# Kernel tuning notes

Measured on AMD Instinct MI355X. Metric: run time of the kernel, lower is better.

Reference implementation:

```python
import jax, jax.numpy as jnp
import numpy as np

B, S, V, L, H, NH, NL = 4, 256, 64, 10, 128, 8, 3
DH = H // NH
LP1 = L + 1


def setup_inputs() -> dict:
    key = jax.random.key(0)
    ks = jax.random.split(key, 18)
    sc = 1.0 / np.sqrt(H)
    return {
        "x": jax.random.normal(ks[0], (B, S, V), jnp.float32),
        "adjacency_logits": jax.random.normal(ks[1], (V, V, LP1), jnp.float32) * 0.1,
        "var_emb": jax.random.normal(ks[2], (V, H), jnp.float32),
        "temp_emb": jax.random.normal(ks[3], (LP1, H), jnp.float32),
        "mech_W": jax.random.normal(ks[4], (V, NL, H, H), jnp.float32) * sc,
        "mech_b": jax.random.normal(ks[5], (V, NL, H), jnp.float32) * 0.01,
        "ln_g": jnp.ones((V, NL, H), jnp.float32),
        "ln_b": jnp.zeros((V, NL, H), jnp.float32),
        "Wq": jax.random.normal(ks[6], (V, H, H), jnp.float32) * sc,
        "Wk": jax.random.normal(ks[7], (V, H, H), jnp.float32) * sc,
        "Wv": jax.random.normal(ks[8], (V, H, H), jnp.float32) * sc,
        "Wo": jax.random.normal(ks[9], (V, H, H), jnp.float32) * sc,
        "bq": jnp.zeros((V, H), jnp.float32),
        "bk": jnp.zeros((V, H), jnp.float32),
        "bv": jnp.zeros((V, H), jnp.float32),
        "bo": jnp.zeros((V, H), jnp.float32),
        "out_W": jax.random.normal(ks[10], (V, H), jnp.float32) * sc,
        "out_b": jnp.zeros((V,), jnp.float32),
    }


def reference(x, adjacency_logits, var_emb, temp_emb, mech_W, mech_b, ln_g, ln_b,
              Wq, Wk, Wv, Wo, bq, bk, bv, bo, out_W, out_b):
    b, s, v = x.shape
    lp1 = adjacency_logits.shape[-1]
    adj = jax.nn.sigmoid(adjacency_logits)  # (V_src, V_tgt, L+1), soft adjacency

    # xlag[b,t,src,l] = x[b, t-l, src] with zero padding (the shift-pad loop, fused)
    xlag = jnp.stack([jnp.pad(x, ((0, 0), (l, 0), (0, 0)))[:, :s] for l in range(lp1)], axis=-1)

    # causal_input[b,t,tgt,h] = sum_{src,l} xlag * adj[src,tgt,l] * (var_emb[src,h] + temp_emb[l,h])
    A = jnp.einsum('btsl,sil->btis', xlag, adj)   # contracted over lag
    Bl = jnp.einsum('btsl,sil->btil', xlag, adj)  # contracted over source
    z = jnp.einsum('btis,sh->btih', A, var_emb) + jnp.einsum('btil,lh->btih', Bl, temp_emb)  # (B,S,V,H)

    # per-variable causal mechanism: Linear -> LayerNorm -> GELU (dropout = identity at eval)
    eps = 1e-5
    nl = mech_W.shape[1]
    for li in range(nl):
        z = jnp.einsum('btvh,vhk->btvk', z, mech_W[:, li]) + mech_b[:, li]
        mu = z.mean(axis=-1, keepdims=True)
        var = z.var(axis=-1, keepdims=True)
        z = (z - mu) / jnp.sqrt(var + eps) * ln_g[:, li] + ln_b[:, li]
        z = jax.nn.gelu(z, approximate=False)

    # per-variable multi-head self-attention over the sequence axis
    def heads(t):
        return t.reshape(b, s, v, NH, DH)
    q = heads(jnp.einsum('btvh,vhk->btvk', z, Wq) + bq)
    k = heads(jnp.einsum('btvh,vhk->btvk', z, Wk) + bk)
    vv = heads(jnp.einsum('btvh,vhk->btvk', z, Wv) + bv)
    scores = jnp.einsum('bqvnd,bkvnd->bvnqk', q, k) / np.sqrt(DH)  # (B,V,NH,S,S)
    attn = jax.nn.softmax(scores, axis=-1)
    o = jnp.einsum('bvnqk,bkvnd->bqvnd', attn, vv).reshape(b, s, v, NH * DH)
    o = jnp.einsum('btvh,vhk->btvk', o, Wo) + bo

    # per-variable output head Linear(H, 1), concatenated over variables
    predictions = jnp.einsum('btvh,vh->btv', o, out_W) + out_b  # (B,S,V)
    return predictions
```

## Files before the change

kernel.cpp:

```cpp
#include <hip/hip_runtime.h>
#include <math.h>

#define BB   4
#define SS   256
#define VV   64
#define LP1  11
#define HH   128
#define NHH  8
#define DHH  16
#define NLL  3
#define BSZ  1024

typedef unsigned short u16;
typedef unsigned int   u32;
typedef __attribute__((ext_vector_type(8))) short s16x8;
typedef __attribute__((ext_vector_type(4))) float f32x4;

__device__ __forceinline__ float bfbits2f(u32 hi16) {
    u32 i = hi16 << 16; float f; __builtin_memcpy(&f, &i, 4); return f;
}
__device__ __forceinline__ u16 f2bf(float f) {
    u32 i; __builtin_memcpy(&i, &f, 4);
    return (u16)((i + 0x7fffu + ((i >> 16) & 1u)) >> 16);
}
__device__ __forceinline__ u16 f2bf_trunc(float f) {
    u32 i; __builtin_memcpy(&i, &f, 4);
    return (u16)(i >> 16);
}
__device__ __forceinline__ float ldf(const void* p, size_t i, int isbf) {
    if (isbf) return bfbits2f(((const u16*)p)[i]);
    return ((const float*)p)[i];
}
__device__ __forceinline__ float4 ld4(const void* p, size_t i, int isbf) {
    float4 v;
    if (isbf) {
        uint2 u = *(const uint2*)((const u16*)p + i);
        v.x = bfbits2f(u.x & 0xffffu); v.y = bfbits2f(u.x >> 16);
        v.z = bfbits2f(u.y & 0xffffu); v.w = bfbits2f(u.y >> 16);
    } else {
        v = *(const float4*)((const float*)p + i);
    }
    return v;
}
__device__ __forceinline__ void gll16(const u16* g, u16* l) {
    __builtin_amdgcn_global_load_lds(
        (const __attribute__((address_space(1))) void*)g,
        (__attribute__((address_space(3))) void*)l, 16, 0, 0);
}

__global__ __launch_bounds__(64) void k_sniff(const u16* __restrict__ probe,
                                              int* __restrict__ flags) {
    if (threadIdx.x == 0) {
        int wild = 0;
        for (int j = 0; j < 256; j++) {
            float v = bfbits2f(probe[j]);
            if (!(fabsf(v) < 1e8f)) wild = 1;
        }
        flags[0] = wild ? 0 : 1;
    }
}

__global__ __launch_bounds__(256) void k_adj(const void* __restrict__ logits,
                                             float* __restrict__ adj,
                                             const int* __restrict__ flags) {
    int isbf = flags[0];
    int i = blockIdx.x * 256 + threadIdx.x;
    if (i < VV * VV * LP1) {
        float v = ldf(logits, i, isbf);
        adj[i] = 1.f / (1.f + expf(-v));
    }
}

__global__ __launch_bounds__(128) void k_fuse(const void* __restrict__ Wo,
                                              const void* __restrict__ outW,
                                              const void* __restrict__ bo,
                                              const void* __restrict__ outb,
                                              float* __restrict__ wfused,
                                              float* __restrict__ bfused,
                                              const int* __restrict__ flags) {
    int isbf = flags[0];
    int v = blockIdx.x; int h = threadIdx.x;
    __shared__ float ow[HH];
    __shared__ float red[HH];
    ow[h] = ldf(outW, (size_t)v * HH + h, isbf);
    __syncthreads();
    size_t wb = ((size_t)v * HH + h) * HH;
    float acc = 0.f;
    #pragma unroll 8
    for (int k = 0; k < HH; k++) acc += ldf(Wo, wb + k, isbf) * ow[k];
    wfused[v * HH + h] = acc;
    red[h] = ldf(bo, (size_t)v * HH + h, isbf) * ow[h];
    __syncthreads();
    for (int s = 64; s > 0; s >>= 1) { if (h < s) red[h] += red[h + s]; __syncthreads(); }
    if (h == 0) bfused[v] = red[0] + ldf(outb, v, isbf);
}

__global__ __launch_bounds__(256) void k_causal(const void* __restrict__ x,
                                                const float* __restrict__ adj,
                                                const void* __restrict__ var_emb,
                                                const void* __restrict__ temp_emb,
                                                u16* __restrict__ zh,
                                                u16* __restrict__ zl,
                                                const int* __restrict__ flags) {
    __shared__ float xl[LP1][VV];
    __shared__ float A_sh[VV][VV + 1];
    __shared__ float Blp_sh[VV * LP1 * 4];
    __shared__ float Bl_sh[VV][12];
    int isbf = flags[0];
    int tid = threadIdx.x;
    int bt = blockIdx.x; int b = bt >> 8; int t = bt & 255;

    for (int p = tid; p < LP1 * VV; p += 256) {
        int l = p >> 6, s = p & 63; int tt = t - l;
        xl[l][s] = (tt >= 0) ? ldf(x, (size_t)(b * SS + tt) * VV + s, isbf) : 0.f;
    }
    __syncthreads();

    {
        int i = tid & 63, sg = tid >> 6;
        float blp[LP1];
        #pragma unroll
        for (int l = 0; l < LP1; l++) blp[l] = 0.f;
        for (int k = 0; k < 16; k++) {
            int s = sg + k * 4;
            const float* ap = adj + (s * VV + i) * LP1;
            float a = 0.f;
            #pragma unroll
            for (int l = 0; l < LP1; l++) {
                float pr = xl[l][s] * ap[l];
                a += pr; blp[l] += pr;
            }
            A_sh[i][s] = a;
        }
        #pragma unroll
        for (int l = 0; l < LP1; l++)
            Blp_sh[(i * LP1 + l) * 4 + sg] = blp[l];
    }
    __syncthreads();
    for (int p = tid; p < VV * LP1; p += 256) {
        int i = p / LP1, l = p - i * LP1;
        const float* q = &Blp_sh[(i * LP1 + l) * 4];
        Bl_sh[i][l] = (q[0] + q[1]) + (q[2] + q[3]);
    }
    __syncthreads();

    int h0 = (tid & 31) * 4;
    int ig = tid >> 5;
    float acc[8][4];
    #pragma unroll
    for (int ii = 0; ii < 8; ii++)
        #pragma unroll
        for (int j = 0; j < 4; j++) acc[ii][j] = 0.f;

    if (isbf) {
        for (int s = 0; s < VV; s++) {
            float4 v4 = ld4(var_emb, (size_t)s * HH + h0, 1);
            #pragma unroll
            for (int ii = 0; ii < 8; ii++) {
                float a = A_sh[ig * 8 + ii][s];
                acc[ii][0] += a * v4.x; acc[ii][1] += a * v4.y;
                acc[ii][2] += a * v4.z; acc[ii][3] += a * v4.w;
            }
        }
        #pragma unroll
        for (int l = 0; l < LP1; l++) {
            float4 t4 = ld4(temp_emb, (size_t)l * HH + h0, 1);
            #pragma unroll
            for (int ii = 0; ii < 8; ii++) {
                float bl = Bl_sh[ig * 8 + ii][l];
                acc[ii][0] += bl * t4.x; acc[ii][1] += bl * t4.y;
                acc[ii][2] += bl * t4.z; acc[ii][3] += bl * t4.w;
            }
        }
    } else {
        for (int s = 0; s < VV; s++) {
            float4 v4 = ld4(var_emb, (size_t)s * HH + h0, 0);
            #pragma unroll
            for (int ii = 0; ii < 8; ii++) {
                float a = A_sh[ig * 8 + ii][s];
                acc[ii][0] += a * v4.x; acc[ii][1] += a * v4.y;
                acc[ii][2] += a * v4.z; acc[ii][3] += a * v4.w;
            }
        }
        #pragma unroll
        for (int l = 0; l < LP1; l++) {
            float4 t4 = ld4(temp_emb, (size_t)l * HH + h0, 0);
            #pragma unroll
            for (int ii = 0; ii < 8; ii++) {
                float bl = Bl_sh[ig * 8 + ii][l];
                acc[ii][0] += bl * t4.x; acc[ii][1] += bl * t4.y;
                acc[ii][2] += bl * t4.z; acc[ii][3] += bl * t4.w;
            }
        }
    }

    #pragma unroll
    for (int ii = 0; ii < 8; ii++) {
        int i = ig * 8 + ii;
        size_t idx = ((size_t)i * BSZ + bt) * HH + h0;
        u16 h0_ = f2bf(acc[ii][0]), h1_ = f2bf(acc[ii][1]);
        u16 h2_ = f2bf(acc[ii][2]), h3_ = f2bf(acc[ii][3]);
        uint2 hw, lw;
        hw.x = (u32)h0_ | ((u32)h1_ << 16); hw.y = (u32)h2_ | ((u32)h3_ << 16);
        lw.x = (u32)f2bf(acc[ii][0] - bfbits2f(h0_)) | ((u32)f2bf(acc[ii][1] - bfbits2f(h1_)) << 16);
        lw.y = (u32)f2bf(acc[ii][2] - bfbits2f(h2_)) | ((u32)f2bf(acc[ii][3] - bfbits2f(h3_)) << 16);
        *(uint2*)&zh[idx] = hw;
        *(uint2*)&zl[idx] = lw;
    }
}

struct WPack {
    const void* src[4];
    u16* dh[4];
    u16* dl[4];
};
#define TP 136
__global__ __launch_bounds__(256) void k_wprep(WPack wp,
                                               const int* __restrict__ flags) {
    int isbf = flags[0];
    int mat = blockIdx.x;
    int seg = (mat < 192) ? 0 : 1 + ((mat - 192) >> 6);
    int rel = (mat < 192) ? mat : ((mat - 192) & 63);
    const void* raw = wp.src[seg];
    u16* Wh = wp.dh[seg];
    u16* Wl = wp.dl[seg];
    int tid = threadIdx.x;
    size_t src = (size_t)rel * (HH * HH);
    if (isbf) {
        __shared__ u16 tile[HH * TP];
        const uint4* sp = (const uint4*)((const u16*)raw + src);
        #pragma unroll
        for (int u = 0; u < 8; u++) {
            int p = u * 256 + tid;
            int h = p >> 4, k8 = (p & 15) * 8;
            int k8s = k8 ^ ((((u32)h >> 3) & 15) * 8);
            *(uint4*)&tile[h * TP + k8s] = sp[p];
        }
        __syncthreads();
        #pragma unroll
        for (int u = 0; u < 8; u++) {
            int p = u * 256 + tid;
            int kcol = p >> 4, h8 = (p & 15) * 8;
            u16 vals[8];
            #pragma unroll
            for (int j = 0; j < 8; j++) {
                int h = h8 + j;
                int ks = kcol ^ ((((u32)h >> 3) & 15) * 8);
                vals[j] = tile[h * TP + ks];
            }
            uint4 pk;
            pk.x = (u32)vals[0] | ((u32)vals[1] << 16);
            pk.y = (u32)vals[2] | ((u32)vals[3] << 16);
            pk.z = (u32)vals[4] | ((u32)vals[5] << 16);
            pk.w = (u32)vals[6] | ((u32)vals[7] << 16);
            int c = h8 >> 6;
            int kloc = (h8 & 63) ^ ((kcol & 7) * 8);
            *(uint4*)&Wh[src + c * 8192 + kcol * 64 + kloc] = pk;
        }
    } else {
        int kcol = tid >> 1, h0 = (tid & 1) * 64;
        for (int i = 0; i < 64; i++) {
            int h = h0 + i;
            float w = ldf(raw, src + (size_t)h * HH + kcol, 0);
            u16 hi = f2bf(w);
            int c = h >> 6;
            size_t dst = src + c * 8192 + (size_t)kcol * 64 + ((h & 63) ^ ((kcol & 7) * 8));
            Wh[dst] = hi;
            Wl[dst] = f2bf(w - bfbits2f(hi));
        }
    }
}

#define PB  72
__global__ __launch_bounds__(256) void k_mega(
    const u16* __restrict__ zh, const u16* __restrict__ zl,
    const u16* __restrict__ WmH, const u16* __restrict__ WmL,
    const u16* __restrict__ WqH, const u16* __restrict__ WqL,
    const u16* __restrict__ WkH, const u16* __restrict__ WkL,
    const u16* __restrict__ WvH, const u16* __restrict__ WvL,
    const void* __restrict__ mechb,
    const void* __restrict__ lng, const void* __restrict__ lnb,
    const void* __restrict__ bq, const void* __restrict__ bk,
    const void* __restrict__ bv,
    u16* __restrict__ Qh, u16* __restrict__ Ql,
    u16* __restrict__ Ko, u16* __restrict__ Vt,
    const int* __restrict__ flags)
{
    __shared__ u16 Az_h[64 * 128];
    __shared__ u16 Az_l[64 * 128];
    __shared__ u16 Bd_s[2][128 * 64];
    u16* Vt_sh = &Bd_s[0][0];
    int isbf = flags[0];
    int wexact = isbf;
    int tid = threadIdx.x;
    int bid = blockIdx.x;
    int xcd = bid & 7, idx = bid >> 3;
    int v = xcd * 8 + (idx >> 4);
    int tile = idx & 15;
    int wave = tid >> 6, lane = tid & 63;
    int quad = lane >> 4, l15 = lane & 15;
    int m0 = wave * 16;
    int swzl = (l15 & 7) * 8;

    size_t zbase = ((size_t)v * BSZ + (size_t)tile * 64) * HH;

    int shift = wexact ? 1 : 2;
    int PER = 1 << shift;
    int NCH = 6 << shift;

    auto wchunk = [&](int ch) -> const u16* {
        int li = ch >> shift;
        int sub = ch & (PER - 1);
        int cc = sub & 1, lo = sub >> 1;
        const u16* p; size_t wb;
        if (li < 3)       { p = lo ? WmL : WmH; wb = (size_t)(v * NLL + li) * 16384; }
        else if (li == 3) { p = lo ? WqL : WqH; wb = (size_t)v * 16384; }
        else if (li == 4) { p = lo ? WkL : WkH; wb = (size_t)v * 16384; }
        else              { p = lo ? WvL : WvH; wb = (size_t)v * 16384; }
        return p + wb + cc * 8192;
    };
    auto stageB = [&](u16* dst, const u16* g) {
        const u16* gl = g + wave * 2048 + lane * 8;
        u16* lb = dst + wave * 2048;
        #pragma unroll
        for (int u = 0; u < 4; u++)
            gll16(gl + u * 512, lb + u * 512);
    };

    {
        int rl = lane >> 4;
        int kc = (lane & 15) * 8;
        #pragma unroll
        for (int u = 0; u < 4; u++) {
            int row = wave * 16 + u * 4 + rl;
            int kcs = kc ^ ((row & 7) * 8);
            gll16(&zh[zbase + (size_t)row * HH + kcs], &Az_h[(wave * 16 + u * 4) * 128]);
            gll16(&zl[zbase + (size_t)row * HH + kcs], &Az_l[(wave * 16 + u * 4) * 128]);
        }
    }
    stageB(&Bd_s[0][0], wchunk(0));
    __syncthreads();

    f32x4 acc[8];

    auto epilogue = [&](int li) {
        float bcol[8], gcol[8], b2col[8];
        #pragma unroll
        for (int nt = 0; nt < 8; nt++) {
            int col = nt * 16 + l15;
            if (li < 3) {
                size_t pb = (size_t)v * (NLL * HH) + (size_t)li * HH + col;
                bcol[nt]  = ldf(mechb, pb, isbf);
                gcol[nt]  = ldf(lng, pb, isbf);
                b2col[nt] = ldf(lnb, pb, isbf);
            } else {
                const void* bp = (li == 3) ? bq : (li == 4) ? bk : bv;
                bcol[nt] = ldf(bp, (size_t)v * HH + col, isbf);
            }
        }
        if (li == 5) __syncthreads();
        #pragma unroll
        for (int r = 0; r < 4; r++) {
            float vals[8];
            float sum = 0.f, sq = 0.f;
            #pragma unroll
            for (int nt = 0; nt < 8; nt++) {
                float val = acc[nt][r] + bcol[nt];
                vals[nt] = val; sum += val; sq += val * val;
            }
            int rloc = m0 + quad * 4 + r;
            if (li < 3) {
                #pragma unroll
                for (int m = 1; m < 16; m <<= 1) {
                    sum += __shfl_xor(sum, m);
                    sq  += __shfl_xor(sq, m);
                }
                float mean = sum * (1.f / HH);
                float var  = sq * (1.f / HH) - mean * mean;
                float rstd = rsqrtf(var + 1e-5f);
                int swr = (rloc & 7) * 8;
                #pragma unroll
                for (int nt = 0; nt < 8; nt++) {
                    float y = (vals[nt] - mean) * rstd * gcol[nt] + b2col[nt];
                    y = 0.5f * y * (1.f + erff(y * 0.70710678118654752f));
                    u16 hi = f2bf(y);
                    int colw = (nt * 16 + l15) ^ swr;
                    Az_h[rloc * 128 + colw] = hi;
                    Az_l[rloc * 128 + colw] = f2bf(y - bfbits2f(hi));
                }
            } else if (li == 3) {
                int row = tile * 64 + rloc;
                size_t ob = ((size_t)v * BSZ + row) * HH;
                #pragma unroll
                for (int nt = 0; nt < 8; nt++) {
                    u16 hi = f2bf(vals[nt]);
                    Qh[ob + nt * 16 + l15] = hi;
                    Ql[ob + nt * 16 + l15] = f2bf(vals[nt] - bfbits2f(hi));
                }
            } else if (li == 4) {
                int row = tile * 64 + rloc;
                size_t ob = ((size_t)v * BSZ + row) * HH;
                #pragma unroll
                for (int nt = 0; nt < 8; nt++)
                    Ko[ob + nt * 16 + l15] = f2bf(vals[nt]);
            } else {
                #pragma unroll
                for (int nt = 0; nt < 8; nt++)
                    Vt_sh[(nt * 16 + l15) * PB + rloc] = f2bf(vals[nt]);
            }
        }
        if (li == 5) {
            __syncthreads();
            int col = tid >> 1, half = tid & 1;
            int n = col >> 4, d = col & 15;
            int bb = tile >> 2, t0 = (tile & 3) * 64;
            size_t dst = (((size_t)(v * BB + bb) * NHH + n) * DHH + d) * SS + t0 + half * 32;
            #pragma unroll
            for (int j = 0; j < 4; j++)
                *(uint4*)&Vt[dst + j * 8] = *(const uint4*)&Vt_sh[col * PB + half * 32 + j * 8];
        }
    };

    for (int ch = 0; ch < NCH; ch++) {
        int bsel = ch & 1;
        if (ch + 1 < NCH) stageB(&Bd_s[bsel ^ 1][0], wchunk(ch + 1));
        int sub = ch & (PER - 1);
        int li = ch >> shift;
        int cc = sub & 1, lo = sub >> 1;
        if (sub == 0) {
            #pragma unroll
            for (int nt = 0; nt < 8; nt++) {
                f32x4 zz = {0.f, 0.f, 0.f, 0.f};
                acc[nt] = zz;
            }
        }
        const u16* Bp = &Bd_s[bsel][0];
        #pragma unroll
        for (int kk = 0; kk < 2; kk++) {
            int acol = (cc * 64 + kk * 32 + quad * 8) ^ swzl;
            int bcol = (kk * 32 + quad * 8) ^ swzl;
            s16x8 ah = *(const s16x8*)&Az_h[(m0 + l15) * 128 + acol];
            if (!lo) {
                s16x8 al = *(const s16x8*)&Az_l[(m0 + l15) * 128 + acol];
                #pragma unroll
                for (int nt = 0; nt < 8; nt++) {
                    s16x8 bh = *(const s16x8*)&Bp[(nt * 16 + l15) * 64 + bcol];
                    acc[nt] = __builtin_amdgcn_mfma_f32_16x16x32_bf16(ah, bh, acc[nt], 0, 0, 0);
                    acc[nt] = __builtin_amdgcn_mfma_f32_16x16x32_bf16(al, bh, acc[nt], 0, 0, 0);
                }
            } else {
                #pragma unroll
                for (int nt = 0; nt < 8; nt++) {
                    s16x8 bl = *(const s16x8*)&Bp[(nt * 16 + l15) * 64 + bcol];
                    acc[nt] = __builtin_amdgcn_mfma_f32_16x16x32_bf16(ah, bl, acc[nt], 0, 0, 0);
                }
            }
        }
        if (sub == PER - 1) epilogue(li);
        __syncthreads();
    }
}

#define LDW 40
__global__ __launch_bounds__(256) void k_attn2(const u16* __restrict__ Qh,
                                               const u16* __restrict__ Ql,
                                               const u16* __restrict__ K16,
                                               const u16* __restrict__ Vt,
                                               float* __restrict__ O) {
    __shared__ u16 Kp_sh[SS * LDW];
    __shared__ u16 Vt_sh[DHH * 264];
    __shared__ u16 P_sh[4][16 * LDW];
    int tid = threadIdx.x;
    int wave = tid >> 6, lane = tid & 63;
    int quad = lane >> 4, l15 = lane & 15;
    int bn = blockIdx.x, v = blockIdx.y;
    int b = bn >> 3, n = bn & 7;
    size_t qkbase = ((size_t)v * BSZ + b * SS) * HH + n * DHH;
    size_t vtbase = ((size_t)(v * BB + b) * NHH + n) * DHH * SS;

    {
        int row = tid;
        uint4 k0 = *(const uint4*)&K16[qkbase + (size_t)row * HH];
        uint4 k1 = *(const uint4*)&K16[qkbase + (size_t)row * HH + 8];
        *(uint4*)&Kp_sh[row * LDW + 0]  = k0;
        *(uint4*)&Kp_sh[row * LDW + 8]  = k1;
        *(uint4*)&Kp_sh[row * LDW + 16] = k0;
        *(uint4*)&Kp_sh[row * LDW + 24] = k1;
    }
    #pragma unroll
    for (int u = 0; u < 2; u++) {
        int p = u * 256 + tid;
        int d = p >> 5, su = (p & 31) * 8;
        *(uint4*)&Vt_sh[d * 264 + su] = *(const uint4*)&Vt[vtbase + (size_t)d * SS + su];
    }
    __syncthreads();

    s16x8 ones;
    #pragma unroll
    for (int i = 0; i < 8; i++) ones[i] = (short)0x3F80;

    for (int mt = wave * 4; mt < wave * 4 + 4; mt++) {
        const u16* Qsrc = (quad < 2) ? Qh : Ql;
        s16x8 aq = *(const s16x8*)&Qsrc[qkbase + (size_t)(mt * 16 + l15) * HH + (quad & 1) * 8];
        f32x4 oacc = {0.f, 0.f, 0.f, 0.f};
        f32x4 lacc = {0.f, 0.f, 0.f, 0.f};
        for (int jt2 = 0; jt2 < 8; jt2++) {
            #pragma unroll
            for (int sub = 0; sub < 2; sub++) {
                int jt = jt2 * 2 + sub;
                s16x8 bk = *(const s16x8*)&Kp_sh[(jt * 16 + l15) * LDW + quad * 8];
                f32x4 s = {0.f, 0.f, 0.f, 0.f};
                s = __builtin_amdgcn_mfma_f32_16x16x32_bf16(aq, bk, s, 0, 0, 0);
                #pragma unroll
                for (int r = 0; r < 4; r++) {
                    float p = __expf(s[r] * 0.25f);
                    P_sh[wave][(quad * 4 + r) * LDW + sub * 16 + l15] = f2bf_trunc(p);
                }
            }
            s16x8 ap = *(const s16x8*)&P_sh[wave][l15 * LDW + quad * 8];
            s16x8 bv = *(const s16x8*)&Vt_sh[l15 * 264 + jt2 * 32 + quad * 8];
            oacc = __builtin_amdgcn_mfma_f32_16x16x32_bf16(ap, bv, oacc, 0, 0, 0);
            lacc = __builtin_amdgcn_mfma_f32_16x16x32_bf16(ap, ones, lacc, 0, 0, 0);
        }
        #pragma unroll
        for (int r = 0; r < 4; r++) {
            float val = oacc[r] / lacc[r];
            O[((size_t)v * BSZ + b * SS + mt * 16 + quad * 4 + r) * HH + n * DHH + l15] = val;
        }
    }
}

__global__ __launch_bounds__(256) void k_final(const float* __restrict__ o,
                                               const float* __restrict__ wfused,
                                               const float* __restrict__ bfused,
                                               void* __restrict__ out,
                                               const int* __restrict__ flags) {
    __shared__ float wf[HH];
    int isbf = flags[0];
    int tid = threadIdx.x; int b = blockIdx.x; int v = blockIdx.y;
    if (tid < HH) wf[tid] = wfused[v * HH + tid];
    __syncthreads();
    int rg = tid >> 3;
    int l8 = tid & 7;
    float4 w0 = *(const float4*)&wf[l8 * 16];
    float4 w1 = *(const float4*)&wf[l8 * 16 + 4];
    float4 w2 = *(const float4*)&wf[l8 * 16 + 8];
    float4 w3 = *(const float4*)&wf[l8 * 16 + 12];
    float bv = bfused[v];
    #pragma unroll
    for (int pass = 0; pass < 8; pass++) {
        int bt = b * SS + pass * 32 + rg;
        const float4* orow = (const float4*)(o + ((size_t)v * BSZ + bt) * HH + l8 * 16);
        float4 a0 = orow[0], a1 = orow[1], a2 = orow[2], a3 = orow[3];
        float acc = a0.x * w0.x + a0.y * w0.y + a0.z * w0.z + a0.w * w0.w
                  + a1.x * w1.x + a1.y * w1.y + a1.z * w1.z + a1.w * w1.w
                  + a2.x * w2.x + a2.y * w2.y + a2.z * w2.z + a2.w * w2.w
                  + a3.x * w3.x + a3.y * w3.y + a3.z * w3.z + a3.w * w3.w;
        acc += __shfl_xor(acc, 1);
        acc += __shfl_xor(acc, 2);
        acc += __shfl_xor(acc, 4);
        if (l8 == 0) {
            float pred = acc + bv;
            size_t oi = (size_t)bt * VV + v;
            if (isbf) ((u16*)out)[oi] = f2bf(pred);
            else      ((float*)out)[oi] = pred;
        }
    }
}

extern "C" void kernel_launch(void* const* d_in, const int* in_sizes, int n_in,
                              void* d_out, int out_size, void* d_ws, size_t ws_size,
                              hipStream_t stream) {
    (void)out_size; (void)ws_size;

    static const int dict_sizes[18]  = {65536,45056,8192,1408,3145728,24576,24576,24576,
                                        1048576,1048576,1048576,1048576,8192,8192,8192,8192,8192,64};
    static const int alpha_sizes[18] = {1048576,1048576,1048576,1048576,45056,8192,8192,8192,
                                        8192,24576,24576,3145728,24576,8192,64,1408,8192,65536};
    static const int alpha_pos[18]   = {17,4,16,15,11,12,10,9,2,0,3,1,7,5,8,6,13,14};
    static const int alpha_logical[18] = {9,11,8,10,1,13,15,12,14,7,6,4,5,16,17,3,2,0};

    const void* in[18];
    bool is_dict = (n_in == 18), is_alpha = (n_in == 18);
    for (int i = 0; i < 18 && i < n_in; i++) {
        if (in_sizes[i] != dict_sizes[i])  is_dict = false;
        if (in_sizes[i] != alpha_sizes[i]) is_alpha = false;
    }
    if (is_dict) {
        for (int i = 0; i < 18; i++) in[i] = d_in[i];
    } else if (is_alpha) {
        for (int i = 0; i < 18; i++) in[i] = d_in[alpha_pos[i]];
    } else {
        bool used[18] = {false};
        for (int a = 0; a < 18; a++) {
            int lg = alpha_logical[a];
            for (int i = 0; i < n_in && i < 18; i++) {
                if (!used[i] && in_sizes[i] == dict_sizes[lg]) {
                    in[lg] = d_in[i]; used[i] = true; break;
                }
            }
        }
    }

    const void* x        = in[0];
    const void* adjl     = in[1];
    const void* var_emb  = in[2];
    const void* temp_emb = in[3];
    const void* mechW    = in[4];
    const void* mechb    = in[5];
    const void* lng      = in[6];
    const void* lnb      = in[7];
    const void* Wq       = in[8];
    const void* Wk       = in[9];
    const void* Wv       = in[10];
    const void* Wo       = in[11];
    const void* bq       = in[12];
    const void* bk       = in[13];
    const void* bv       = in[14];
    const void* bo       = in[15];
    const void* outW     = in[16];
    const void* outb     = in[17];

    float* ws     = (float*)d_ws;
    int*   flags  = (int*)ws;
    float* adj    = ws + 32;
    float* wfused = ws + 45088;
    float* bfused = ws + 53280;
    u16*   zhA    = (u16*)(ws + 53376);
    u16*   zlA    = (u16*)(ws + 4247680);
    u16*   zhB    = (u16*)(ws + 8441984);
    u16*   zlB    = (u16*)(ws + 12636288);
    float* Obuf   = ws + 53376;
    u16*   K16    = (u16*)(ws + 16830592);
    u16*   Vt16   = (u16*)(ws + 21024896);
    u16*   WtmH   = (u16*)(ws + 25219200);
    u16*   WtmL   = (u16*)(ws + 26792064);
    u16*   WtqH   = (u16*)(ws + 28364928);
    u16*   WtqL   = (u16*)(ws + 28889216);
    u16*   WtkH   = (u16*)(ws + 29413504);
    u16*   WtkL   = (u16*)(ws + 29937792);
    u16*   WtvH   = (u16*)(ws + 30462080);
    u16*   WtvL   = (u16*)(ws + 30986368);

    k_sniff <<<dim3(1),    dim3(64),  0, stream>>>((const u16*)mechW, flags);
    k_adj   <<<dim3(176),  dim3(256), 0, stream>>>(adjl, adj, flags);
    k_fuse  <<<dim3(64),   dim3(128), 0, stream>>>(Wo, outW, bo, outb, wfused, bfused, flags);

    WPack wp;
    wp.src[0] = mechW; wp.dh[0] = WtmH; wp.dl[0] = WtmL;
    wp.src[1] = Wq;    wp.dh[1] = WtqH; wp.dl[1] = WtqL;
    wp.src[2] = Wk;    wp.dh[2] = WtkH; wp.dl[2] = WtkL;
    wp.src[3] = Wv;    wp.dh[3] = WtvH; wp.dl[3] = WtvL;
    k_wprep <<<dim3(384),  dim3(256), 0, stream>>>(wp, flags);

    k_causal<<<dim3(BSZ),  dim3(256), 0, stream>>>(x, adj, var_emb, temp_emb, zhA, zlA, flags);

    k_mega<<<dim3(1024), dim3(256), 0, stream>>>(
            zhA, zlA,
            WtmH, WtmL, WtqH, WtqL, WtkH, WtkL, WtvH, WtvL,
            mechb, lng, lnb, bq, bk, bv,
            zhB, zlB, K16, Vt16, flags);

    k_attn2 <<<dim3(BB * NHH, VV), dim3(256), 0, stream>>>(zhB, zlB, K16, Vt16, Obuf);
    k_final <<<dim3(BB, VV), dim3(256), 0, stream>>>(Obuf, wfused, bfused, d_out, flags);
}
```

Measured before the change: 420.5 us.

## Fuse causal-input computation into mega kernel using MFMA embedding projection

```diff
diff --git a/kernel.cpp b/kernel.cpp
--- a/kernel.cpp
+++ b/kernel.cpp
@@ -26,6 +26,11 @@
 __device__ __forceinline__ u16 f2bf_trunc(float f) {
     u32 i; __builtin_memcpy(&i, &f, 4);
     return (u16)(i >> 16);
+}
+__device__ __forceinline__ u32 cvtpk(float lo, float hi) {
+    u32 r;
+    asm("v_cvt_pk_bf16_f32 %0, %1, %2" : "=v"(r) : "v"(lo), "v"(hi));
+    return r;
 }
 __device__ __forceinline__ float ldf(const void* p, size_t i, int isbf) {
     if (isbf) return bfbits2f(((const u16*)p)[i]);
@@ -95,136 +100,53 @@
     if (h == 0) bfused[v] = red[0] + ldf(outb, v, isbf);
 }
 
-__global__ __launch_bounds__(256) void k_causal(const void* __restrict__ x,
-                                                const float* __restrict__ adj,
-                                                const void* __restrict__ var_emb,
-                                                const void* __restrict__ temp_emb,
-                                                u16* __restrict__ zh,
-                                                u16* __restrict__ zl,
-                                                const int* __restrict__ flags) {
-    __shared__ float xl[LP1][VV];
-    __shared__ float A_sh[VV][VV + 1];
-    __shared__ float Blp_sh[VV * LP1 * 4];
-    __shared__ float Bl_sh[VV][12];
-    int isbf = flags[0];
-    int tid = threadIdx.x;
-    int bt = blockIdx.x; int b = bt >> 8; int t = bt & 255;
-
-    for (int p = tid; p < LP1 * VV; p += 256) {
-        int l = p >> 6, s = p & 63; int tt = t - l;
-        xl[l][s] = (tt >= 0) ? ldf(x, (size_t)(b * SS + tt) * VV + s, isbf) : 0.f;
-    }
-    __syncthreads();
-
-    {
-        int i = tid & 63, sg = tid >> 6;
-        float blp[LP1];
-        #pragma unroll
-        for (int l = 0; l < LP1; l++) blp[l] = 0.f;
-        for (int k = 0; k < 16; k++) {
-            int s = sg + k * 4;
-            const float* ap = adj + (s * VV + i) * LP1;
-            float a = 0.f;
-            #pragma unroll
-            for (int l = 0; l < LP1; l++) {
-                float pr = xl[l][s] * ap[l];
-                a += pr; blp[l] += pr;
-            }
-            A_sh[i][s] = a;
-        }
-        #pragma unroll
-        for (int l = 0; l < LP1; l++)
-            Blp_sh[(i * LP1 + l) * 4 + sg] = blp[l];
-    }
-    __syncthreads();
-    for (int p = tid; p < VV * LP1; p += 256) {
-        int i = p / LP1, l = p - i * LP1;
-        const float* q = &Blp_sh[(i * LP1 + l) * 4];
-        Bl_sh[i][l] = (q[0] + q[1]) + (q[2] + q[3]);
-    }
-    __syncthreads();
-
-    int h0 = (tid & 31) * 4;
-    int ig = tid >> 5;
-    float acc[8][4];
-    #pragma unroll
-    for (int ii = 0; ii < 8; ii++)
-        #pragma unroll
-        for (int j = 0; j < 4; j++) acc[ii][j] = 0.f;
-
-    if (isbf) {
-        for (int s = 0; s < VV; s++) {
-            float4 v4 = ld4(var_emb, (size_t)s * HH + h0, 1);
-            #pragma unroll
-            for (int ii = 0; ii < 8; ii++) {
-                float a = A_sh[ig * 8 + ii][s];
-                acc[ii][0] += a * v4.x; acc[ii][1] += a * v4.y;
-                acc[ii][2] += a * v4.z; acc[ii][3] += a * v4.w;
-            }
-        }
-        #pragma unroll
-        for (int l = 0; l < LP1; l++) {
-            float4 t4 = ld4(temp_emb, (size_t)l * HH + h0, 1);
-            #pragma unroll
-            for (int ii = 0; ii < 8; ii++) {
-                float bl = Bl_sh[ig * 8 + ii][l];
-                acc[ii][0] += bl * t4.x; acc[ii][1] += bl * t4.y;
-                acc[ii][2] += bl * t4.z; acc[ii][3] += bl * t4.w;
-            }
-        }
-    } else {
-        for (int s = 0; s < VV; s++) {
-            float4 v4 = ld4(var_emb, (size_t)s * HH + h0, 0);
-            #pragma unroll
-            for (int ii = 0; ii < 8; ii++) {
-                float a = A_sh[ig * 8 + ii][s];
-                acc[ii][0] += a * v4.x; acc[ii][1] += a * v4.y;
-                acc[ii][2] += a * v4.z; acc[ii][3] += a * v4.w;
-            }
-        }
-        #pragma unroll
-        for (int l = 0; l < LP1; l++) {
-            float4 t4 = ld4(temp_emb, (size_t)l * HH + h0, 0);
-            #pragma unroll
-            for (int ii = 0; ii < 8; ii++) {
-                float bl = Bl_sh[ig * 8 + ii][l];
-                acc[ii][0] += bl * t4.x; acc[ii][1] += bl * t4.y;
-                acc[ii][2] += bl * t4.z; acc[ii][3] += bl * t4.w;
-            }
-        }
-    }
-
-    #pragma unroll
-    for (int ii = 0; ii < 8; ii++) {
-        int i = ig * 8 + ii;
-        size_t idx = ((size_t)i * BSZ + bt) * HH + h0;
-        u16 h0_ = f2bf(acc[ii][0]), h1_ = f2bf(acc[ii][1]);
-        u16 h2_ = f2bf(acc[ii][2]), h3_ = f2bf(acc[ii][3]);
-        uint2 hw, lw;
-        hw.x = (u32)h0_ | ((u32)h1_ << 16); hw.y = (u32)h2_ | ((u32)h3_ << 16);
-        lw.x = (u32)f2bf(acc[ii][0] - bfbits2f(h0_)) | ((u32)f2bf(acc[ii][1] - bfbits2f(h1_)) << 16);
-        lw.y = (u32)f2bf(acc[ii][2] - bfbits2f(h2_)) | ((u32)f2bf(acc[ii][3] - bfbits2f(h3_)) << 16);
-        *(uint2*)&zh[idx] = hw;
-        *(uint2*)&zl[idx] = lw;
-    }
-}
-
 struct WPack {
-    const void* src[4];
-    u16* dh[4];
-    u16* dl[4];
+    const void* src[6];
+    u16* dh[6];
+    u16* dl[6];
 };
 #define TP 136
 __global__ __launch_bounds__(256) void k_wprep(WPack wp,
                                                const int* __restrict__ flags) {
     int isbf = flags[0];
     int mat = blockIdx.x;
+    int tid = threadIdx.x;
+    if (mat >= 384) {
+        if (mat == 384) {
+            const void* raw = wp.src[4];
+            u16* dh = wp.dh[4]; u16* dl = wp.dl[4];
+            int n = tid >> 1, half = tid & 1;
+            for (int i = 0; i < 32; i++) {
+                int s = half * 32 + i;
+                float val = ldf(raw, (size_t)s * HH + n, isbf);
+                u16 hi = f2bf(val);
+                int dst = n * 64 + (s ^ ((n & 7) * 8));
+                dh[dst] = hi;
+                dl[dst] = f2bf(val - bfbits2f(hi));
+            }
+        } else {
+            const void* raw = wp.src[5];
+            u16* dh = wp.dh[5]; u16* dl = wp.dl[5];
+            for (int p = tid; p < 8192; p += 256) { dh[p] = 0; dl[p] = 0; }
+            __syncthreads();
+            if (tid < HH) {
+                int n = tid;
+                for (int l = 0; l < LP1; l++) {
+                    float val = ldf(raw, (size_t)l * HH + n, isbf);
+                    u16 hi = f2bf(val);
+                    int dst = n * 64 + (l ^ ((n & 7) * 8));
+                    dh[dst] = hi;
+                    dl[dst] = f2bf(val - bfbits2f(hi));
+                }
+            }
+        }
+        return;
+    }
     int seg = (mat < 192) ? 0 : 1 + ((mat - 192) >> 6);
     int rel = (mat < 192) ? mat : ((mat - 192) & 63);
     const void* raw = wp.src[seg];
     u16* Wh = wp.dh[seg];
     u16* Wl = wp.dl[seg];
-    int tid = threadIdx.x;
     size_t src = (size_t)rel * (HH * HH);
     if (isbf) {
         __shared__ u16 tile[HH * TP];
@@ -273,7 +195,9 @@
 
 #define PB  72
 __global__ __launch_bounds__(256) void k_mega(
-    const u16* __restrict__ zh, const u16* __restrict__ zl,
+    const void* __restrict__ x, const float* __restrict__ adjp,
+    const u16* __restrict__ VeH, const u16* __restrict__ VeL,
+    const u16* __restrict__ TeH, const u16* __restrict__ TeL,
     const u16* __restrict__ WmH, const u16* __restrict__ WmL,
     const u16* __restrict__ WqH, const u16* __restrict__ WqL,
     const u16* __restrict__ WkH, const u16* __restrict__ WkL,
@@ -286,10 +210,12 @@
     u16* __restrict__ Ko, u16* __restrict__ Vt,
     const int* __restrict__ flags)
 {
-    __shared__ u16 Az_h[64 * 128];
-    __shared__ u16 Az_l[64 * 128];
-    __shared__ u16 Bd_s[2][128 * 64];
-    u16* Vt_sh = &Bd_s[0][0];
+    __shared__ __align__(16) u16 SMEM[32768];
+    u16* Az_h = SMEM;
+    u16* Az_l = SMEM + 8192;
+    u16* BdS  = SMEM + 16384;
+    u16* Vt_sh = BdS;
+
     int isbf = flags[0];
     int wexact = isbf;
     int tid = threadIdx.x;
@@ -297,12 +223,176 @@
     int xcd = bid & 7, idx = bid >> 3;
     int v = xcd * 8 + (idx >> 4);
     int tile = idx & 15;
+    int b = tile >> 2, t0 = (tile & 3) * 64;
     int wave = tid >> 6, lane = tid & 63;
     int quad = lane >> 4, l15 = lane & 15;
     int m0 = wave * 16;
     int swzl = (l15 & 7) * 8;
 
-    size_t zbase = ((size_t)v * BSZ + (size_t)tile * 64) * HH;
+    float* xt = (float*)SMEM;
+    for (int p = tid; p < 74 * 64; p += 256) {
+        int rr = p >> 6, s = p & 63;
+        int trow = t0 - 10 + rr;
+        float val = (trow >= 0) ? ldf(x, (size_t)(b * SS + trow) * VV + s, isbf) : 0.f;
+        xt[s * 81 + rr] = val;
+    }
+    __syncthreads();
+
+    float* A_f = (float*)BdS;
+    float* Blp = A_f + 64 * 68;
+    float* Blf = Blp + 64 * 44;
+    {
+        int t = lane;
+        int sg = wave;
+        float blp[LP1];
+        #pragma unroll
+        for (int l = 0; l < LP1; l++) blp[l] = 0.f;
+        for (int k = 0; k < 16; k++) {
+            int s = sg * 16 + k;
+            const float* ap = adjp + (s * VV + v) * LP1;
+            float xw[LP1];
+            #pragma unroll
+            for (int j = 0; j < LP1; j++) xw[j] = xt[s * 81 + t + j];
+            float a = 0.f;
+            #pragma unroll
+            for (int l = 0; l < LP1; l++) {
+                float pr = xw[10 - l] * ap[l];
+                a += pr; blp[l] += pr;
+            }
+            A_f[t * 68 + s] = a;
+        }
+        #pragma unroll
+        for (int l = 0; l < LP1; l++) Blp[t * 44 + sg * 11 + l] = blp[l];
+    }
+    __syncthreads();
+    {
+        int t = tid >> 2, c0 = (tid & 3) * 4;
+        #pragma unroll
+        for (int c = c0; c < c0 + 4; c++) {
+            float s4 = 0.f;
+            if (c < LP1)
+                s4 = (Blp[t * 44 + c] + Blp[t * 44 + 11 + c]) +
+                     (Blp[t * 44 + 22 + c] + Blp[t * 44 + 33 + c]);
+            Blf[t * 16 + c] = s4;
+        }
+    }
+    __syncthreads();
+
+    s16x8 ahf[2], alf[2], blh, bll;
+    #pragma unroll
+    for (int kk = 0; kk < 2; kk++) {
+        #pragma unroll
+        for (int j = 0; j < 8; j++) {
+            float a = A_f[(m0 + l15) * 68 + kk * 32 + quad * 8 + j];
+            u32 w = cvtpk(a, a);
+            u16 hi = (u16)(w & 0xffffu);
+            ahf[kk][j] = (short)hi;
+            float res = a - bfbits2f(hi);
+            alf[kk][j] = (short)(cvtpk(res, res) & 0xffffu);
+        }
+    }
+    #pragma unroll
+    for (int j = 0; j < 8; j++) {
+        float a = (quad < 2) ? Blf[(m0 + l15) * 16 + quad * 8 + j] : 0.f;
+        u32 w = cvtpk(a, a);
+        u16 hi = (u16)(w & 0xffffu);
+        blh[j] = (short)hi;
+        float res = a - bfbits2f(hi);
+        bll[j] = (short)(cvtpk(res, res) & 0xffffu);
+    }
+    __syncthreads();
+
+    auto stageB = [&](u16* dst, const u16* g) {
+        const u16* gl = g + wave * 2048 + lane * 8;
+        u16* lb = dst + wave * 2048;
+        #pragma unroll
+        for (int u = 0; u < 4; u++)
+            gll16(gl + u * 512, lb + u * 512);
+    };
+
+    f32x4 acc[8];
+    #pragma unroll
+    for (int nt = 0; nt < 8; nt++) {
+        f32x4 zz = {0.f, 0.f, 0.f, 0.f};
+        acc[nt] = zz;
+    }
+
+    if (wexact) {
+        stageB(BdS, VeH);
+        stageB(BdS + 8192, TeH);
+        __syncthreads();
+        #pragma unroll
+        for (int kk = 0; kk < 2; kk++) {
+            int bcol = (kk * 32 + quad * 8) ^ swzl;
+            #pragma unroll
+            for (int nt = 0; nt < 8; nt++) {
+                s16x8 bh = *(const s16x8*)&BdS[(nt * 16 + l15) * 64 + bcol];
+                acc[nt] = __builtin_amdgcn_mfma_f32_16x16x32_bf16(ahf[kk], bh, acc[nt], 0, 0, 0);
+                acc[nt] = __builtin_amdgcn_mfma_f32_16x16x32_bf16(alf[kk], bh, acc[nt], 0, 0, 0);
+            }
+        }
+        {
+            int bcol = (quad * 8) ^ swzl;
+            #pragma unroll
+            for (int nt = 0; nt < 8; nt++) {
+                s16x8 th = *(const s16x8*)&BdS[8192 + (nt * 16 + l15) * 64 + bcol];
+                acc[nt] = __builtin_amdgcn_mfma_f32_16x16x32_bf16(blh, th, acc[nt], 0, 0, 0);
+                acc[nt] = __builtin_amdgcn_mfma_f32_16x16x32_bf16(bll, th, acc[nt], 0, 0, 0);
+            }
+        }
+    } else {
+        stageB(BdS, VeH);
+        stageB(BdS + 8192, VeL);
+        __syncthreads();
+        #pragma unroll
+        for (int kk = 0; kk < 2; kk++) {
+            int bcol = (kk * 32 + quad * 8) ^ swzl;
+            #pragma unroll
+            for (int nt = 0; nt < 8; nt++) {
+                s16x8 bh = *(const s16x8*)&BdS[(nt * 16 + l15) * 64 + bcol];
+                s16x8 bl = *(const s16x8*)&BdS[8192 + (nt * 16 + l15) * 64 + bcol];
+                acc[nt] = __builtin_amdgcn_mfma_f32_16x16x32_bf16(ahf[kk], bh, acc[nt], 0, 0, 0);
+                acc[nt] = __builtin_amdgcn_mfma_f32_16x16x32_bf16(alf[kk], bh, acc[nt], 0, 0, 0);
+                acc[nt] = __builtin_amdgcn_mfma_f32_16x16x32_bf16(ahf[kk], bl, acc[nt], 0, 0, 0);
+            }
+        }
+        __syncthreads();
+        stageB(BdS, TeH);
+        stageB(BdS + 8192, TeL);
+        __syncthreads();
+        {
+            int bcol = (quad * 8) ^ swzl;
+            #pragma unroll
+            for (int nt = 0; nt < 8; nt++) {
+                s16x8 th = *(const s16x8*)&BdS[(nt * 16 + l15) * 64 + bcol];
+                s16x8 tl = *(const s16x8*)&BdS[8192 + (nt * 16 + l15) * 64 + bcol];
+                acc[nt] = __builtin_amdgcn_mfma_f32_16x16x32_bf16(blh, th, acc[nt], 0, 0, 0);
+                acc[nt] = __builtin_amdgcn_mfma_f32_16x16x32_bf16(bll, th, acc[nt], 0, 0, 0);
+                acc[nt] = __builtin_amdgcn_mfma_f32_16x16x32_bf16(blh, tl, acc[nt], 0, 0, 0);
+            }
+        }
+    }
+    __syncthreads();
+
+    #pragma unroll
+    for (int r = 0; r < 4; r++) {
+        int rloc = m0 + quad * 4 + r;
+        int swr = (rloc & 7) * 8;
+        #pragma unroll
+        for (int nt = 0; nt < 8; nt++) {
+            float val = acc[nt][r];
+            float sx = __shfl_xor(val, 1);
+            u32 w = cvtpk(val, sx);
+            float res = val - bfbits2f(w & 0xffffu);
+            float rx = __shfl_xor(res, 1);
+            u32 wl = cvtpk(res, rx);
+            if (!(l15 & 1)) {
+                int colw = (nt * 16 + (l15 & ~1)) ^ swr;
+                *(u32*)&Az_h[rloc * 128 + colw] = w;
+                *(u32*)&Az_l[rloc * 128 + colw] = wl;
+            }
+        }
+    }
 
     int shift = wexact ? 1 : 2;
     int PER = 1 << shift;
@@ -319,29 +409,6 @@
         else              { p = lo ? WvL : WvH; wb = (size_t)v * 16384; }
         return p + wb + cc * 8192;
     };
-    auto stageB = [&](u16* dst, const u16* g) {
-        const u16* gl = g + wave * 2048 + lane * 8;
-        u16* lb = dst + wave * 2048;
-        #pragma unroll
-        for (int u = 0; u < 4; u++)
-            gll16(gl + u * 512, lb + u * 512);
-    };
-
-    {
-        int rl = lane >> 4;
-        int kc = (lane & 15) * 8;
-        #pragma unroll
-        for (int u = 0; u < 4; u++) {
-            int row = wave * 16 + u * 4 + rl;
-            int kcs = kc ^ ((row & 7) * 8);
-            gll16(&zh[zbase + (size_t)row * HH + kcs], &Az_h[(wave * 16 + u * 4) * 128]);
-            gll16(&zl[zbase + (size_t)row * HH + kcs], &Az_l[(wave * 16 + u * 4) * 128]);
-        }
-    }
-    stageB(&Bd_s[0][0], wchunk(0));
-    __syncthreads();
-
-    f32x4 acc[8];
 
     auto epilogue = [&](int li) {
         float bcol[8], gcol[8], b2col[8];
@@ -383,26 +450,44 @@
                 for (int nt = 0; nt < 8; nt++) {
                     float y = (vals[nt] - mean) * rstd * gcol[nt] + b2col[nt];
                     y = 0.5f * y * (1.f + erff(y * 0.70710678118654752f));
-                    u16 hi = f2bf(y);
-                    int colw = (nt * 16 + l15) ^ swr;
-                    Az_h[rloc * 128 + colw] = hi;
-                    Az_l[rloc * 128 + colw] = f2bf(y - bfbits2f(hi));
+                    float sx = __shfl_xor(y, 1);
+                    u32 w = cvtpk(y, sx);
+                    float res = y - bfbits2f(w & 0xffffu);
+                    float rx = __shfl_xor(res, 1);
+                    u32 wl = cvtpk(res, rx);
+                    if (!(l15 & 1)) {
+                        int colw = (nt * 16 + (l15 & ~1)) ^ swr;
+                        *(u32*)&Az_h[rloc * 128 + colw] = w;
+                        *(u32*)&Az_l[rloc * 128 + colw] = wl;
+                    }
                 }
             } else if (li == 3) {
                 int row = tile * 64 + rloc;
                 size_t ob = ((size_t)v * BSZ + row) * HH;
                 #pragma unroll
                 for (int nt = 0; nt < 8; nt++) {
-                    u16 hi = f2bf(vals[nt]);
-                    Qh[ob + nt * 16 + l15] = hi;
-                    Ql[ob + nt * 16 + l15] = f2bf(vals[nt] - bfbits2f(hi));
+                    float val = vals[nt];
+                    float sx = __shfl_xor(val, 1);
+                    u32 w = cvtpk(val, sx);
+                    float res = val - bfbits2f(w & 0xffffu);
+                    float rx = __shfl_xor(res, 1);
+                    u32 wl = cvtpk(res, rx);
+                    if (!(l15 & 1)) {
+                        size_t oi = ob + nt * 16 + (l15 & ~1);
+                        *(u32*)&Qh[oi] = w;
+                        *(u32*)&Ql[oi] = wl;
+                    }
                 }
             } else if (li == 4) {
                 int row = tile * 64 + rloc;
                 size_t ob = ((size_t)v * BSZ + row) * HH;
                 #pragma unroll
-                for (int nt = 0; nt < 8; nt++)
-                    Ko[ob + nt * 16 + l15] = f2bf(vals[nt]);
+                for (int nt = 0; nt < 8; nt++) {
+                    u32 h = f2bf(vals[nt]);
+                    u32 hx = (u32)__shfl_xor((int)h, 1);
+                    if (!(l15 & 1))
+                        *(u32*)&Ko[ob + nt * 16 + (l15 & ~1)] = h | (hx << 16);
+                }
             } else {
                 #pragma unroll
                 for (int nt = 0; nt < 8; nt++)
@@ -413,17 +498,20 @@
             __syncthreads();
             int col = tid >> 1, half = tid & 1;
             int n = col >> 4, d = col & 15;
-            int bb = tile >> 2, t0 = (tile & 3) * 64;
-            size_t dst = (((size_t)(v * BB + bb) * NHH + n) * DHH + d) * SS + t0 + half * 32;
+            int bb = tile >> 2, tq = (tile & 3) * 64;
+            size_t dst = (((size_t)(v * BB + bb) * NHH + n) * DHH + d) * SS + tq + half * 32;
             #pragma unroll
             for (int j = 0; j < 4; j++)
                 *(uint4*)&Vt[dst + j * 8] = *(const uint4*)&Vt_sh[col * PB + half * 32 + j * 8];
         }
     };
 
+    stageB(BdS, wchunk(0));
+    __syncthreads();
+
     for (int ch = 0; ch < NCH; ch++) {
         int bsel = ch & 1;
-        if (ch + 1 < NCH) stageB(&Bd_s[bsel ^ 1][0], wchunk(ch + 1));
+        if (ch + 1 < NCH) stageB(BdS + (bsel ^ 1) * 8192, wchunk(ch + 1));
         int sub = ch & (PER - 1);
         int li = ch >> shift;
         int cc = sub & 1, lo = sub >> 1;
@@ -434,7 +522,7 @@
                 acc[nt] = zz;
             }
         }
-        const u16* Bp = &Bd_s[bsel][0];
+        const u16* Bp = BdS + bsel * 8192;
         #pragma unroll
         for (int kk = 0; kk < 2; kk++) {
             int acol = (cc * 64 + kk * 32 + quad * 8) ^ swzl;
@@ -626,11 +714,9 @@
     float* adj    = ws + 32;
     float* wfused = ws + 45088;
     float* bfused = ws + 53280;
-    u16*   zhA    = (u16*)(ws + 53376);
-    u16*   zlA    = (u16*)(ws + 4247680);
+    float* Obuf   = ws + 53376;
     u16*   zhB    = (u16*)(ws + 8441984);
     u16*   zlB    = (u16*)(ws + 12636288);
-    float* Obuf   = ws + 53376;
     u16*   K16    = (u16*)(ws + 16830592);
     u16*   Vt16   = (u16*)(ws + 21024896);
     u16*   WtmH   = (u16*)(ws + 25219200);
@@ -641,22 +727,27 @@
     u16*   WtkL   = (u16*)(ws + 29937792);
     u16*   WtvH   = (u16*)(ws + 30462080);
     u16*   WtvL   = (u16*)(ws + 30986368);
+    u16*   WveH   = (u16*)(ws + 31510656);
+    u16*   WveL   = (u16*)(ws + 31514752);
+    u16*   WteH   = (u16*)(ws + 31518848);
+    u16*   WteL   = (u16*)(ws + 31522944);
 
     k_sniff <<<dim3(1),    dim3(64),  0, stream>>>((const u16*)mechW, flags);
     k_adj   <<<dim3(176),  dim3(256), 0, stream>>>(adjl, adj, flags);
     k_fuse  <<<dim3(64),   dim3(128), 0, stream>>>(Wo, outW, bo, outb, wfused, bfused, flags);
 
     WPack wp;
-    wp.src[0] = mechW; wp.dh[0] = WtmH; wp.dl[0] = WtmL;
-    wp.src[1] = Wq;    wp.dh[1] = WtqH; wp.dl[1] = WtqL;
-    wp.src[2] = Wk;    wp.dh[2] = WtkH; wp.dl[2] = WtkL;
-    wp.src[3] = Wv;    wp.dh[3] = WtvH; wp.dl[3] = WtvL;
-    k_wprep <<<dim3(384),  dim3(256), 0, stream>>>(wp, flags);
-
-    k_causal<<<dim3(BSZ),  dim3(256), 0, stream>>>(x, adj, var_emb, temp_emb, zhA, zlA, flags);
+    wp.src[0] = mechW;    wp.dh[0] = WtmH; wp.dl[0] = WtmL;
+    wp.src[1] = Wq;       wp.dh[1] = WtqH; wp.dl[1] = WtqL;
+    wp.src[2] = Wk;       wp.dh[2] = WtkH; wp.dl[2] = WtkL;
+    wp.src[3] = Wv;       wp.dh[3] = WtvH; wp.dl[3] = WtvL;
+    wp.src[4] = var_emb;  wp.dh[4] = WveH; wp.dl[4] = WveL;
+    wp.src[5] = temp_emb; wp.dh[5] = WteH; wp.dl[5] = WteL;
+    k_wprep <<<dim3(386),  dim3(256), 0, stream>>>(wp, flags);
 
     k_mega<<<dim3(1024), dim3(256), 0, stream>>>(
-            zhA, zlA,
+            x, adj,
+            WveH, WveL, WteH, WteL,
             WtmH, WtmL, WtqH, WtqL, WtkH, WtkL, WtvH, WtvL,
             mechb, lng, lnb, bq, bk, bv,
             zhB, zlB, K16, Vt16, flags);
```

New measurement: 403.0 us. -4.2%, faster.
